# Kernel tuning notes

Hardware: AMD Instinct MI355X
Metric: run time of the kernel (lower is better)

Reference implementation:

```python
import jax, jax.numpy as jnp
import numpy as np

# ---- module hyperparameters (from init_kwargs) ----
DIST = 25
N_IN, N_HID, N_OUT = 16, 128, 2
D_MODEL, D_STATE, D_CONV, EXPAND, HEADDIM = 256, 64, 4, 2, 64
D_INNER = EXPAND * D_MODEL            # 512
NHEADS = D_INNER // HEADDIM           # 8
CONV_DIM = D_INNER + 2 * D_STATE      # 640 (x, B, C share the conv)
D_IN_PROJ = 2 * D_INNER + 2 * D_STATE + NHEADS  # 1160
NUM_CHECK = DIST ** 2 - 1             # 624 (mamba seq len)
NPG = NUM_CHECK + DIST ** 2           # 1249 nodes per graph
BATCH = 64
N_NODES = BATCH * NPG                 # 79936
N_EDGES = N_NODES * 8                 # 639488


def setup_inputs() -> dict:
    key = jax.random.key(0)
    ks = jax.random.split(key, 16)
    w = lambda k, shape, s=0.02: jax.random.normal(k, shape, jnp.float32) * s
    return {
        "node_inputs": jax.random.normal(ks[0], (N_NODES, N_IN), jnp.float32),
        "src_ids": jax.random.randint(ks[1], (N_EDGES,), 0, N_NODES),
        "dst_ids": jax.random.randint(ks[2], (N_EDGES,), 0, N_NODES),
        "W_embed": w(ks[3], (N_IN, D_MODEL)), "b_embed": jnp.zeros((D_MODEL,), jnp.float32),
        "W_in": w(ks[4], (D_MODEL, D_IN_PROJ)), "b_in": jnp.zeros((D_IN_PROJ,), jnp.float32),
        "conv_w": w(ks[5], (CONV_DIM, D_CONV), 0.1), "conv_b": jnp.zeros((CONV_DIM,), jnp.float32),
        "A_log": jnp.log(jnp.arange(1, NHEADS + 1, dtype=jnp.float32)),
        "dt_bias": w(ks[6], (NHEADS,), 0.1),
        "D_skip": jnp.ones((NHEADS,), jnp.float32),
        "norm_w": jnp.ones((D_INNER,), jnp.float32),
        "W_outp": w(ks[7], (D_INNER, D_MODEL)), "b_outp": jnp.zeros((D_MODEL,), jnp.float32),
        "W_proj": w(ks[8], (D_MODEL, N_IN)), "b_proj": jnp.zeros((N_IN,), jnp.float32),
        "W_msg": w(ks[9], (N_IN, N_HID)), "b_msg": jnp.zeros((N_HID,), jnp.float32),
        "W_upd": w(ks[10], (N_IN + N_HID, N_HID)), "b_upd": jnp.zeros((N_HID,), jnp.float32),
        "W_out": w(ks[11], (N_HID, N_OUT)), "b_out": jnp.zeros((N_OUT,), jnp.float32),
    }


def _silu(x):
    return x * jax.nn.sigmoid(x)


def _mamba2(x, W_in, b_in, conv_w, conv_b, A_log, dt_bias, D_skip, norm_w, W_outp, b_outp):
    """Mamba2 block: in_proj -> causal depthwise conv -> selective scan -> gated RMSNorm -> out_proj."""
    Bg, L, _ = x.shape
    zxbcdt = x @ W_in + b_in                       # [Bg, L, 1160]
    z = zxbcdt[..., :D_INNER]                      # gate
    xBC = zxbcdt[..., D_INNER:D_INNER + CONV_DIM]
    dt = zxbcdt[..., D_INNER + CONV_DIM:]          # [Bg, L, H]
    # causal depthwise conv over the seq dim (d_conv taps)
    xp = jnp.pad(xBC, ((0, 0), (D_CONV - 1, 0), (0, 0)))
    xBC = sum(conv_w[:, k] * xp[:, k:k + L, :] for k in range(D_CONV)) + conv_b
    xBC = _silu(xBC)
    xs = xBC[..., :D_INNER].reshape(Bg, L, NHEADS, HEADDIM)
    Bm = xBC[..., D_INNER:D_INNER + D_STATE]       # [Bg, L, N] (ngroups=1)
    Cm = xBC[..., D_INNER + D_STATE:]              # [Bg, L, N]
    dt = jax.nn.softplus(dt + dt_bias)             # [Bg, L, H]
    dA = jnp.exp(dt * (-jnp.exp(A_log)))           # [Bg, L, H]

    def step(h, inp):
        xt, Bt, Ct, dAt, dtt = inp                 # xt [Bg,H,P], Bt/Ct [Bg,N], dAt/dtt [Bg,H]
        h = dAt[..., None, None] * h + dtt[..., None, None] * xt[..., None] * Bt[:, None, None, :]
        yt = jnp.einsum('bhpn,bn->bhp', h, Ct)
        return h, yt

    h0 = jnp.zeros((Bg, NHEADS, HEADDIM, D_STATE), x.dtype)
    seq = (jnp.moveaxis(xs, 1, 0), jnp.moveaxis(Bm, 1, 0), jnp.moveaxis(Cm, 1, 0),
           jnp.moveaxis(dA, 1, 0), jnp.moveaxis(dt, 1, 0))
    _, ys = jax.lax.scan(step, h0, seq)
    ys = jnp.moveaxis(ys, 1, 0) + xs * D_skip[None, None, :, None]   # [Bg, L, H, P]
    y = ys.reshape(Bg, L, D_INNER) * _silu(z)                        # gated
    y = y * jax.lax.rsqrt(jnp.mean(y * y, axis=-1, keepdims=True) + 1e-5) * norm_w
    return y @ W_outp + b_outp


def reference(node_inputs, src_ids, dst_ids, W_embed, b_embed, W_in, b_in, conv_w, conv_b,
              A_log, dt_bias, D_skip, norm_w, W_outp, b_outp, W_proj, b_proj,
              W_msg, b_msg, W_upd, b_upd, W_out, b_out):
    # gather check-node rows: i*nodes_per_graph + j for j < num_check
    idx = (jnp.arange(BATCH)[:, None] * NPG + jnp.arange(NUM_CHECK)[None, :]).reshape(-1)
    chk = node_inputs[idx]                                           # [B*624, 16]
    emb = (chk @ W_embed + b_embed).reshape(BATCH, NUM_CHECK, D_MODEL)
    y = _mamba2(emb, W_in, b_in, conv_w, conv_b, A_log, dt_bias, D_skip, norm_w, W_outp, b_outp)
    proj = y.reshape(-1, D_MODEL) @ W_proj + b_proj                  # [B*624, 16]
    # scatter back into zero tensor at check-node slots
    feat = jnp.zeros((node_inputs.shape[0], N_IN), node_inputs.dtype).at[idx].set(proj)
    # GNN message passing: gather src, transform, scatter-sum into dst, update, readout
    msg = jax.nn.relu(feat[src_ids] @ W_msg + b_msg)                 # [E, n_hidden]
    agg = jax.ops.segment_sum(msg, dst_ids, num_segments=feat.shape[0])
    h = jax.nn.relu(jnp.concatenate([feat, agg], axis=-1) @ W_upd + b_upd)
    return h @ W_out + b_out                                         # [N, n_node_outputs]
```

## Files before the change

### kernel.cpp

```cpp
#include <hip/hip_runtime.h>
#include <math.h>

#define LSEQ 624
#define NPG_C 1249
#define BATCH_C 64
#define NROWS (BATCH_C*LSEQ)
#define N_NODES_C 79936
#define N_EDGES_C 639488
#define DIP 1160
#define DIN 512
#define CDIM 640
#define NH 8
#define HD 64
#define DS 64
#define CAP 96
#define TCH 48
#define NCHK 13
#define HSLOT 2097152

#define OFF_CHK   0
#define OFF_WF    638976
#define OFF_BF    657536
#define OFF_WOP   658944
#define OFF_BOP   667136
#define OFF_XBC   667392
#define OFF_DTV   26226432
#define OFF_EV    26545920
#define OFF_YS    26865408
#define OFF_FEAT  47312640
#define OFF_AGG   48591616
#define OFF_ECUM  (OFF_AGG + 2000000)
#define OFF_BBF   (OFF_AGG + 2400000)
#define OFF_PROJ  (OFF_XBC + 8000000)

typedef __attribute__((ext_vector_type(8))) short bf16x8;
typedef __attribute__((ext_vector_type(4))) float f32x4;

__device__ __forceinline__ float siluf(float x) {
    return x / (1.f + __expf(-x));
}

__device__ __forceinline__ unsigned short f2bf(float f) {
    unsigned int u = __float_as_uint(f);
    u += 0x7fffu + ((u >> 16) & 1u);
    return (unsigned short)(u >> 16);
}
__device__ __forceinline__ float bf2f(unsigned short h) {
    return __uint_as_float(((unsigned int)h) << 16);
}

__device__ __forceinline__ unsigned short* hstp(unsigned short* hst, int c, int b, int head) {
    return hst + (size_t)(c - 1) * HSLOT + (size_t)(b * NH + head) * 4096;
}

__global__ void k_gather(const float* __restrict__ ni, float* __restrict__ chk) {
    int gid = blockIdx.x * 256 + threadIdx.x;
    if (gid >= NROWS * 16) return;
    int row = gid >> 4, k = gid & 15;
    int node = (row / LSEQ) * NPG_C + (row % LSEQ);
    chk[gid] = ni[node * 16 + k];
}

__global__ void k_fusew(const float* __restrict__ We, const float* __restrict__ be,
                        const float* __restrict__ Wi, const float* __restrict__ bi,
                        const float* __restrict__ Wo, const float* __restrict__ bo,
                        const float* __restrict__ Wp, const float* __restrict__ bp,
                        float* __restrict__ Wf, float* __restrict__ bf,
                        float* __restrict__ Wop, float* __restrict__ bop) {
    int id = blockIdx.x * 256 + threadIdx.x;
    if (id < 16 * DIP) {
        int i = id / DIP, j = id % DIP;
        float s = 0.f;
        for (int k = 0; k < 256; k++) s = fmaf(We[i * 256 + k], Wi[k * DIP + j], s);
        Wf[id] = s;
    } else if (id < 16 * DIP + DIP) {
        int j = id - 16 * DIP;
        float s = bi[j];
        for (int k = 0; k < 256; k++) s = fmaf(be[k], Wi[k * DIP + j], s);
        bf[j] = s;
    } else if (id < 16 * DIP + DIP + DIN * 16) {
        int id2 = id - (16 * DIP + DIP);
        int c = id2 >> 4, o = id2 & 15;
        float s = 0.f;
        for (int k = 0; k < 256; k++) s = fmaf(Wo[c * 256 + k], Wp[k * 16 + o], s);
        Wop[id2] = s;
    } else if (id < 16 * DIP + DIP + DIN * 16 + 16) {
        int o = id - (16 * DIP + DIP + DIN * 16);
        float s = bp[o];
        for (int k = 0; k < 256; k++) s = fmaf(bo[k], Wp[k * 16 + o], s);
        bop[o] = s;
    }
}

__global__ __launch_bounds__(320) void k_conv(const float* __restrict__ chk,
        const float* __restrict__ Wf, const float* __restrict__ bf,
        const float* __restrict__ cw, const float* __restrict__ cb,
        float* __restrict__ xBCc, unsigned short* __restrict__ bbf) {
    int c = blockIdx.x * 320 + threadIdx.x;
    int t0 = blockIdx.y * 78;
    int b = blockIdx.z;
    float w[16];
#pragma unroll
    for (int k = 0; k < 16; k++) w[k] = Wf[k * DIP + DIN + c];
    float bfx = bf[DIN + c];
    float k0 = cw[c * 4 + 0], k1 = cw[c * 4 + 1], k2 = cw[c * 4 + 2], k3 = cw[c * 4 + 3];
    float cbv = cb[c];
    const float* crow = chk + (size_t)(b * LSEQ) * 16;
    float* out = xBCc + (size_t)(b * LSEQ) * CDIM + c;
    int isB = (c >= 512 && c < 576);
    unsigned short* bout = bbf + (size_t)(b * LSEQ) * 64 + (c - 512);

    float w0 = 0.f, w1 = 0.f, w2 = 0.f;
#pragma unroll
    for (int d = 3; d >= 1; d--) {
        int tau = t0 - d;
        float s = 0.f;
        if (tau >= 0) {
            s = bfx;
            const float* cr = crow + tau * 16;
#pragma unroll
            for (int k = 0; k < 16; k++) s = fmaf(cr[k], w[k], s);
        }
        if (d == 3) w0 = s; else if (d == 2) w1 = s; else w2 = s;
    }
    for (int t = t0; t < t0 + 78; t++) {
        const float* cr = crow + t * 16;
        float w3 = bfx;
#pragma unroll
        for (int k = 0; k < 16; k++) w3 = fmaf(cr[k], w[k], w3);
        float a = fmaf(k0, w0, fmaf(k1, w1, fmaf(k2, w2, fmaf(k3, w3, cbv))));
        float v = siluf(a);
        out[(size_t)t * CDIM] = v;
        if (isB) bout[(size_t)t * 64] = f2bf(v);
        w0 = w1; w1 = w2; w2 = w3;
    }
}

__global__ __launch_bounds__(256) void k_dte(const float* __restrict__ chk,
        const float* __restrict__ Wf, const float* __restrict__ bf,
        const float* __restrict__ A_log, const float* __restrict__ dt_bias,
        float* __restrict__ dtv, float* __restrict__ ecum) {
    int s = blockIdx.x * 4 + (threadIdx.x >> 6);
    int lane = threadIdx.x & 63;
    int h = s & 7;
    int cb = s >> 3;
    int c = cb % NCHK, b = cb / NCHK;
    int r0 = b * LSEQ + c * TCH;
    float wcol[16];
#pragma unroll
    for (int k = 0; k < 16; k++) wcol[k] = Wf[k * DIP + DIN + CDIM + h];
    float base = bf[DIN + CDIM + h] + dt_bias[h];
    float nA = -__expf(A_log[h]);
    float v = 0.f, sp = 0.f;
    if (lane < TCH) {
        const float* cr = chk + (size_t)(r0 + lane) * 16;
        float acc = base;
#pragma unroll
        for (int k = 0; k < 16; k++) acc = fmaf(cr[k], wcol[k], acc);
        sp = (acc > 20.f) ? acc : log1pf(__expf(acc));
        v = nA * sp;
    }
#pragma unroll
    for (int off = 1; off < 64; off <<= 1) {
        float u = __shfl_up(v, off);
        if (lane >= off) v += u;
    }
    if (lane < TCH) {
        dtv[(size_t)(r0 + lane) * NH + h] = sp;
        ecum[(size_t)(r0 + lane) * NH + h] = v;
    }
}

__global__ __launch_bounds__(256) void k_gmat(const float* __restrict__ xBCc,
        float* __restrict__ Gm) {
    int c = blockIdx.x, b = blockIdx.y;
    int tid = threadIdx.x;
    int bs = b * LSEQ;
    __shared__ __align__(16) float sBC[TCH * 132];
#pragma unroll
    for (int j = 0; j < 6; j++) {
        int g = j * 256 + tid;
        int f = g * 4;
        int t = f >> 7, col = f & 127;
        float4 v = *(const float4*)(xBCc + (size_t)(bs + c * TCH + t) * CDIM + 512 + col);
        *(float4*)&sBC[t * 132 + col] = v;
    }
    __syncthreads();
    int t0 = (tid >> 4) * 3, s0 = (tid & 15) * 3;
    float acc[3][3];
#pragma unroll
    for (int i = 0; i < 3; i++)
#pragma unroll
        for (int j = 0; j < 3; j++) acc[i][j] = 0.f;
    for (int k = 0; k < 64; k++) {
        float c0 = sBC[(t0 + 0) * 132 + 64 + k];
        float c1 = sBC[(t0 + 1) * 132 + 64 + k];
        float c2 = sBC[(t0 + 2) * 132 + 64 + k];
        float b0 = sBC[(s0 + 0) * 132 + k];
        float b1 = sBC[(s0 + 1) * 132 + k];
        float b2 = sBC[(s0 + 2) * 132 + k];
        acc[0][0] = fmaf(c0, b0, acc[0][0]); acc[0][1] = fmaf(c0, b1, acc[0][1]); acc[0][2] = fmaf(c0, b2, acc[0][2]);
        acc[1][0] = fmaf(c1, b0, acc[1][0]); acc[1][1] = fmaf(c1, b1, acc[1][1]); acc[1][2] = fmaf(c1, b2, acc[1][2]);
        acc[2][0] = fmaf(c2, b0, acc[2][0]); acc[2][1] = fmaf(c2, b1, acc[2][1]); acc[2][2] = fmaf(c2, b2, acc[2][2]);
    }
    size_t gb = (size_t)(b * NCHK + c) * (TCH * TCH);
#pragma unroll
    for (int i = 0; i < 3; i++)
#pragma unroll
        for (int j = 0; j < 3; j++)
            Gm[gb + (t0 + i) * TCH + (s0 + j)] = acc[i][j];
}

__global__ __launch_bounds__(256) void k_scarry(const float* __restrict__ xBCc,
        const unsigned short* __restrict__ bbf,
        const float* __restrict__ dtv, const float* __restrict__ ecum,
        unsigned short* __restrict__ hst) {
    int head = blockIdx.x, b = blockIdx.y;
    int pz = blockIdx.z * 32;
    int tid = threadIdx.x;
    int bs = b * LSEQ;
    __shared__ __align__(16) float sX[TCH * 32];
    __shared__ __align__(16) float sB[TCH * 64];
    __shared__ float sW[TCH];

    int i2 = (tid >> 4) * 2;
    int j4 = (tid & 15) * 4;

    float h[2][4];
#pragma unroll
    for (int i = 0; i < 2; i++)
#pragma unroll
        for (int j = 0; j < 4; j++) h[i][j] = 0.f;

    float4 rX0, rX1;
    ushort4 rBu[3];
    float rEc = 0.f, rDt = 0.f, rEcL = 0.f;

#define SC_ISSUE(cc)                                                                \
    {                                                                               \
        int r0i = bs + (cc) * TCH;                                                  \
        {   int f = 4 * tid; int t = f >> 5; int col = f & 31;                      \
            rX0 = *(const float4*)(xBCc + (size_t)(r0i + t) * CDIM + head * HD + pz + col); \
            if (tid < 128) {                                                        \
                int f2 = 1024 + 4 * tid; int t2 = f2 >> 5; int col2 = f2 & 31;      \
                rX1 = *(const float4*)(xBCc + (size_t)(r0i + t2) * CDIM + head * HD + pz + col2); \
            }                                                                       \
        }                                                                           \
        _Pragma("unroll")                                                           \
        for (int jj = 0; jj < 3; jj++) {                                            \
            int g = jj * 256 + tid; int f = 4 * g; int t = f >> 6; int col = f & 63;\
            rBu[jj] = *(const ushort4*)(bbf + (size_t)(r0i + t) * 64 + col);        \
        }                                                                           \
        if (tid < TCH) { rEc = ecum[(size_t)(r0i + tid) * NH + head];               \
                         rDt = dtv[(size_t)(r0i + tid) * NH + head]; }              \
        rEcL = ecum[(size_t)(r0i + TCH - 1) * NH + head];                           \
    }

    SC_ISSUE(0);
    for (int c = 0; c < NCHK; c++) {
        __syncthreads();
        float eL = __expf(rEcL);
        {
            int f = 4 * tid;
            *(float4*)&sX[f] = rX0;
            if (tid < 128) *(float4*)&sX[1024 + f] = rX1;
        }
#pragma unroll
        for (int jj = 0; jj < 3; jj++) {
            int g = jj * 256 + tid;
            float4 bv = { bf2f(rBu[jj].x), bf2f(rBu[jj].y), bf2f(rBu[jj].z), bf2f(rBu[jj].w) };
            *(float4*)&sB[4 * g] = bv;
        }
        if (tid < TCH) sW[tid] = __expf(rEcL - rEc) * rDt;
        __syncthreads();
        if (c + 1 < NCHK) SC_ISSUE(c + 1);

        if (c > 0) {
            unsigned short* hp = hstp(hst, c, b, head);
#pragma unroll
            for (int ii = 0; ii < 2; ii++) {
                ushort4 v = { f2bf(h[ii][0]), f2bf(h[ii][1]), f2bf(h[ii][2]), f2bf(h[ii][3]) };
                *(ushort4*)&hp[(pz + i2 + ii) * 64 + j4] = v;
            }
        }

#pragma unroll
        for (int i = 0; i < 2; i++)
#pragma unroll
            for (int j = 0; j < 4; j++) h[i][j] *= eL;
        for (int s = 0; s < TCH; s++) {
            float w = sW[s];
            float2 xv = *(const float2*)&sX[s * 32 + i2];
            float4 bv = *(const float4*)&sB[s * 64 + j4];
            float x0 = w * xv.x, x1 = w * xv.y;
            h[0][0] = fmaf(x0, bv.x, h[0][0]); h[0][1] = fmaf(x0, bv.y, h[0][1]);
            h[0][2] = fmaf(x0, bv.z, h[0][2]); h[0][3] = fmaf(x0, bv.w, h[0][3]);
            h[1][0] = fmaf(x1, bv.x, h[1][0]); h[1][1] = fmaf(x1, bv.y, h[1][1]);
            h[1][2] = fmaf(x1, bv.z, h[1][2]); h[1][3] = fmaf(x1, bv.w, h[1][3]);
        }
    }
#undef SC_ISSUE
}

__global__ __launch_bounds__(256) void k_intra(float* __restrict__ xBCc,
        const float* __restrict__ Gm, const float* __restrict__ dtv,
        const float* __restrict__ ecum, const float* __restrict__ Dskip,
        const unsigned short* __restrict__ hst) {
    int bid = blockIdx.x;
    int xcd = bid & 7;
    int head = (bid >> 3) & 7;
    int g = (bid >> 6) * 8 + xcd;
    int c = g % NCHK, b = g / NCHK;
    int tid = threadIdx.x;
    int lane = tid & 63;
    int wv = tid >> 6;
    int bs = b * LSEQ;
    int r0 = bs + c * TCH;

    __shared__ __align__(16) unsigned char smraw[35904];
    float* sXf = (float*)(smraw);
    unsigned short* sMh = (unsigned short*)(smraw + 12288);
    unsigned short* sMl = (unsigned short*)(smraw + 19200);
    unsigned short* sCt = (unsigned short*)(smraw + 19200);
    unsigned short* sXh = (unsigned short*)(smraw + 26112);
    unsigned short* sHt = (unsigned short*)(smraw + 26112);
    float* sE  = (float*)(smraw + 35328);
    float* sEx = (float*)(smraw + 35520);
    float* sdt = (float*)(smraw + 35712);

    ushort4 rHu[4];
    if (c > 0) {
        const unsigned short* hp = hstp((unsigned short*)hst, c, b, head);
#pragma unroll
        for (int j = 0; j < 4; j++)
            rHu[j] = *(const ushort4*)(hp + 4 * (j * 256 + tid));
    }

    ushort4 rCu[3];
#pragma unroll
    for (int j = 0; j < 3; j++) {
        int g2 = j * 256 + tid;
        int t = g2 >> 4, col = (g2 & 15) * 4;
        const float* rowp = xBCc + (size_t)(r0 + t) * CDIM;
        float4 xv = *(const float4*)(rowp + head * HD + col);
        *(float4*)&sXf[t * 64 + col] = xv;
        float4 cv = *(const float4*)(rowp + 576 + col);
        ushort4 cu = { f2bf(cv.x), f2bf(cv.y), f2bf(cv.z), f2bf(cv.w) };
        rCu[j] = cu;
    }
    if (tid < TCH) {
        float e = ecum[(size_t)(r0 + tid) * NH + head];
        sE[tid] = e;
        sEx[tid] = __expf(e);
        sdt[tid] = dtv[(size_t)(r0 + tid) * NH + head];
    }
    __syncthreads();

    size_t gb = (size_t)(b * NCHK + c) * (TCH * TCH);
#pragma unroll
    for (int k = 0; k < 9; k++) {
        int id = k * 256 + tid;
        int t = id / TCH, s = id - t * TCH;
        float gv = Gm[gb + id];
        float m = (s <= t) ? __expf(sE[t] - sE[s]) * sdt[s] * gv : 0.f;
        unsigned short mh = f2bf(m);
        sMh[t * 72 + s] = mh;
        sMl[t * 72 + s] = f2bf(m - bf2f(mh));
    }
    for (int w = tid; w < 768; w += 256) {
        int t = w >> 4, s = 48 + (w & 15);
        sMh[t * 72 + s] = 0;
        sMl[t * 72 + s] = 0;
    }
#pragma unroll
    for (int i = 0; i < 3; i++) {
        int w = i * 256 + tid;
        int p = w & 63, k4 = (w >> 6) * 4;
        float v0 = sXf[(k4 + 0) * 64 + p];
        float v1 = sXf[(k4 + 1) * 64 + p];
        float v2 = sXf[(k4 + 2) * 64 + p];
        float v3 = sXf[(k4 + 3) * 64 + p];
        ushort4 hi = { f2bf(v0), f2bf(v1), f2bf(v2), f2bf(v3) };
        *(ushort4*)&sXh[p * 72 + k4] = hi;
    }
    {
        int p = tid >> 2, k4 = 48 + (tid & 3) * 4;
        ushort4 z = { 0, 0, 0, 0 };
        *(ushort4*)&sXh[p * 72 + k4] = z;
    }
    __syncthreads();

    int pt = wv * 16;
    int colL = lane & 15;
    int rbase = (lane >> 4) * 4;
    int kfrag = 8 * (lane >> 4);

    float xo[3][4];
#pragma unroll
    for (int tt = 0; tt < 3; tt++)
#pragma unroll
        for (int r = 0; r < 4; r++)
            xo[tt][r] = sXf[(tt * 16 + rbase + r) * 64 + pt + colL];

    f32x4 acc[3] = { {0,0,0,0}, {0,0,0,0}, {0,0,0,0} };
    f32x4 acc2[3] = { {0,0,0,0}, {0,0,0,0}, {0,0,0,0} };
#pragma unroll
    for (int ks = 0; ks < 64; ks += 32) {
        bf16x8 bh = *(const bf16x8*)&sXh[(pt + colL) * 72 + ks + kfrag];
#pragma unroll
        for (int tt = 0; tt < 3; tt++) {
            bf16x8 ah = *(const bf16x8*)&sMh[(tt * 16 + colL) * 72 + ks + kfrag];
            bf16x8 al = *(const bf16x8*)&sMl[(tt * 16 + colL) * 72 + ks + kfrag];
            acc[tt] = __builtin_amdgcn_mfma_f32_16x16x32_bf16(ah, bh, acc[tt], 0, 0, 0);
            acc[tt] = __builtin_amdgcn_mfma_f32_16x16x32_bf16(al, bh, acc[tt], 0, 0, 0);
        }
    }
    __syncthreads();
#pragma unroll
    for (int j = 0; j < 3; j++) {
        int g2 = j * 256 + tid;
        int t = g2 >> 4, col = (g2 & 15) * 4;
        *(ushort4*)&sCt[t * 72 + col] = rCu[j];
    }
    if (c > 0) {
#pragma unroll
        for (int j = 0; j < 4; j++) {
            int e = 4 * (j * 256 + tid);
            int p = e >> 6, n4 = e & 63;
            *(ushort4*)&sHt[p * 72 + n4] = rHu[j];
        }
    }
    __syncthreads();
    if (c > 0) {
#pragma unroll
        for (int ks = 0; ks < 64; ks += 32) {
            bf16x8 bhh = *(const bf16x8*)&sHt[(pt + colL) * 72 + ks + kfrag];
#pragma unroll
            for (int tt = 0; tt < 3; tt++) {
                bf16x8 ac = *(const bf16x8*)&sCt[(tt * 16 + colL) * 72 + ks + kfrag];
                acc2[tt] = __builtin_amdgcn_mfma_f32_16x16x32_bf16(ac, bhh, acc2[tt], 0, 0, 0);
            }
        }
    }

    float dsk = Dskip[head];
#pragma unroll
    for (int tt = 0; tt < 3; tt++) {
#pragma unroll
        for (int r = 0; r < 4; r++) {
            int trow = tt * 16 + rbase + r;
            float y = fmaf(dsk, xo[tt][r], acc[tt][r]);
            if (c > 0) y = fmaf(sEx[trow], acc2[tt][r], y);
            xBCc[(size_t)(r0 + trow) * CDIM + head * HD + pt + colL] = y;
        }
    }
}

__global__ __launch_bounds__(256) void k_gate(const float* __restrict__ chk,
        const float* __restrict__ Wf, const float* __restrict__ bf,
        const float* __restrict__ ysx, const float* __restrict__ norm_w,
        const float* __restrict__ Wop, const float* __restrict__ bop,
        float* __restrict__ feat) {
    int row0 = blockIdx.x * 8;
    int tid = threadIdx.x;
    __shared__ float sy[2][512];
    __shared__ float sred[2][256];
    __shared__ float swave[2][4];
    int c1 = tid, c2 = tid + 256;
    float wz1[16], wz2[16];
#pragma unroll
    for (int k = 0; k < 16; k++) {
        wz1[k] = Wf[k * DIP + c1];
        wz2[k] = Wf[k * DIP + c2];
    }
    float zb1 = bf[c1], zb2 = bf[c2];
    float nw1 = norm_w[c1], nw2 = norm_w[c2];
    int o = tid & 15, kg = tid >> 4;
    int wid = tid >> 6, lane = tid & 63;

    for (int g2 = 0; g2 < 4; g2++) {
        int rb = row0 + g2 * 2;
        float gn1[2], gn2[2];
#pragma unroll
        for (int r = 0; r < 2; r++) {
            int row = rb + r;
            const float4* cp = (const float4*)(chk + (size_t)row * 16);
            float4 cA = cp[0], cB = cp[1], cC = cp[2], cD = cp[3];
            float cv[16] = {cA.x,cA.y,cA.z,cA.w, cB.x,cB.y,cB.z,cB.w,
                            cC.x,cC.y,cC.z,cC.w, cD.x,cD.y,cD.z,cD.w};
            float z1 = zb1, z2 = zb2;
#pragma unroll
            for (int k = 0; k < 16; k++) {
                z1 = fmaf(cv[k], wz1[k], z1);
                z2 = fmaf(cv[k], wz2[k], z2);
            }
            float y1 = ysx[(size_t)row * CDIM + c1] * siluf(z1);
            float y2 = ysx[(size_t)row * CDIM + c2] * siluf(z2);
            gn1[r] = y1;
            gn2[r] = y2;
            float ss = y1 * y1 + y2 * y2;
#pragma unroll
            for (int off = 32; off >= 1; off >>= 1) ss += __shfl_xor(ss, off);
            if (lane == 0) swave[r][wid] = ss;
        }
        __syncthreads();
#pragma unroll
        for (int r = 0; r < 2; r++) {
            float tot = swave[r][0] + swave[r][1] + swave[r][2] + swave[r][3];
            float scale = 1.f / sqrtf(tot * (1.f / 512.f) + 1e-5f);
            sy[r][c1] = gn1[r] * scale * nw1;
            sy[r][c2] = gn2[r] * scale * nw2;
        }
        __syncthreads();
#pragma unroll
        for (int r = 0; r < 2; r++) {
            float ps = 0.f;
#pragma unroll
            for (int j = 0; j < 32; j++) {
                int k = kg * 32 + j;
                ps = fmaf(sy[r][k], Wop[k * 16 + o], ps);
            }
            sred[r][kg * 16 + o] = ps;
        }
        __syncthreads();
        if (tid < 32) {
            int r = tid >> 4, oo = tid & 15;
            float s = bop[oo];
#pragma unroll
            for (int g = 0; g < 16; g++) s += sred[r][g * 16 + oo];
            int row = rb + r;
            int bb = row / LSEQ, t = row % LSEQ;
            feat[(size_t)(bb * NPG_C + t) * 16 + oo] = s;
        }
    }
}

__global__ void k_scatter(const int* __restrict__ src, const int* __restrict__ dst,
                          int* __restrict__ cnt, int* __restrict__ slots) {
    int e = blockIdx.x * 256 + threadIdx.x;
    if (e >= N_EDGES_C) return;
    int d = dst[e];
    int pos = atomicAdd(&cnt[d], 1);
    if (pos < CAP) slots[(size_t)d * CAP + pos] = src[e];
}

__global__ __launch_bounds__(256) void k_proj(const float* __restrict__ feat,
        const float* __restrict__ Wm, const float* __restrict__ bm,
        unsigned short* __restrict__ p) {
    int tid = threadIdx.x;
    int c = tid & 127, half = tid >> 7;
    float w[16];
#pragma unroll
    for (int k = 0; k < 16; k++) w[k] = Wm[k * 128 + c];
    float bmv = bm[c];
    int base = blockIdx.x * 8;
#pragma unroll
    for (int q = 0; q < 4; q++) {
        int node = base + q * 2 + half;
        const float4* fr = (const float4*)(feat + (size_t)node * 16);
        float4 f0 = fr[0], f1 = fr[1], f2 = fr[2], f3 = fr[3];
        float m = bmv;
        m = fmaf(f0.x, w[0],  m); m = fmaf(f0.y, w[1],  m);
        m = fmaf(f0.z, w[2],  m); m = fmaf(f0.w, w[3],  m);
        m = fmaf(f1.x, w[4],  m); m = fmaf(f1.y, w[5],  m);
        m = fmaf(f1.z, w[6],  m); m = fmaf(f1.w, w[7],  m);
        m = fmaf(f2.x, w[8],  m); m = fmaf(f2.y, w[9],  m);
        m = fmaf(f2.z, w[10], m); m = fmaf(f2.w, w[11], m);
        m = fmaf(f3.x, w[12], m); m = fmaf(f3.y, w[13], m);
        m = fmaf(f3.z, w[14], m); m = fmaf(f3.w, w[15], m);
        p[(size_t)node * 128 + c] = f2bf(fmaxf(m, 0.f));
    }
}

__global__ __launch_bounds__(256) void k_agg2(const int* __restrict__ cnt,
        const int* __restrict__ slots, const unsigned short* __restrict__ p,
        float* __restrict__ agg) {
    int wid = threadIdx.x >> 6, lane = threadIdx.x & 63;
    int esub = lane >> 4, cl = lane & 15;
    int d = blockIdx.x * 4 + wid;
    int deg = cnt[d];
    if (deg > CAP) deg = CAP;
    const int* sl = slots + (size_t)d * CAP;

    float acc[8];
#pragma unroll
    for (int j = 0; j < 8; j++) acc[j] = 0.f;

    int e = esub;
    int s = (e < deg) ? sl[e] : -1;
    while (e < deg) {
        int scur = s;
        int en = e + 4;
        if (en < deg) s = sl[en];
        ushort4 v0, v1;
        {
            const unsigned short* pp = p + (size_t)scur * 128 + cl * 8;
            v0 = *(const ushort4*)(pp);
            v1 = *(const ushort4*)(pp + 4);
        }
        acc[0] += bf2f(v0.x); acc[1] += bf2f(v0.y);
        acc[2] += bf2f(v0.z); acc[3] += bf2f(v0.w);
        acc[4] += bf2f(v1.x); acc[5] += bf2f(v1.y);
        acc[6] += bf2f(v1.z); acc[7] += bf2f(v1.w);
        e = en;
    }
#pragma unroll
    for (int j = 0; j < 8; j++) {
        acc[j] += __shfl_xor(acc[j], 16);
        acc[j] += __shfl_xor(acc[j], 32);
    }
    if (esub == 0) {
        float4 o0 = { acc[0], acc[1], acc[2], acc[3] };
        float4 o1 = { acc[4], acc[5], acc[6], acc[7] };
        float* ap = agg + (size_t)d * 128 + cl * 8;
        *(float4*)(ap) = o0;
        *(float4*)(ap + 4) = o1;
    }
}

#define UNB 32
__global__ __launch_bounds__(256) void k_upd2(const float* __restrict__ feat,
        const float* __restrict__ agg, const float* __restrict__ Wu,
        const float* __restrict__ bu, const float* __restrict__ Wo2,
        const float* __restrict__ bo2, float* __restrict__ out) {
    int g0 = blockIdx.x * UNB;
    int tid = threadIdx.x;
    __shared__ __align__(16) float sin_[UNB][144];
    __shared__ float part[4][8][2];
    for (int w = tid; w < UNB * 144; w += 256) {
        int node = w / 144, k = w - node * 144;
        sin_[node][k] = (k < 16) ? feat[(size_t)(g0 + node) * 16 + k]
                                 : agg[(size_t)(g0 + node) * 128 + (k - 16)];
    }
    __syncthreads();
    int c6 = tid & 63;
    int grp = tid >> 6;
    float acc[8][2];
#pragma unroll
    for (int nn = 0; nn < 8; nn++) { acc[nn][0] = 0.f; acc[nn][1] = 0.f; }

    for (int k0 = 0; k0 < 144; k0 += 4) {
        float wA0 = Wu[(k0 + 0) * 128 + c6], wB0 = Wu[(k0 + 0) * 128 + 64 + c6];
        float wA1 = Wu[(k0 + 1) * 128 + c6], wB1 = Wu[(k0 + 1) * 128 + 64 + c6];
        float wA2 = Wu[(k0 + 2) * 128 + c6], wB2 = Wu[(k0 + 2) * 128 + 64 + c6];
        float wA3 = Wu[(k0 + 3) * 128 + c6], wB3 = Wu[(k0 + 3) * 128 + 64 + c6];
#pragma unroll
        for (int nn = 0; nn < 8; nn++) {
            float4 s4 = *(const float4*)&sin_[grp * 8 + nn][k0];
            acc[nn][0] = fmaf(s4.x, wA0, acc[nn][0]);
            acc[nn][1] = fmaf(s4.x, wB0, acc[nn][1]);
            acc[nn][0] = fmaf(s4.y, wA1, acc[nn][0]);
            acc[nn][1] = fmaf(s4.y, wB1, acc[nn][1]);
            acc[nn][0] = fmaf(s4.z, wA2, acc[nn][0]);
            acc[nn][1] = fmaf(s4.z, wB2, acc[nn][1]);
            acc[nn][0] = fmaf(s4.w, wA3, acc[nn][0]);
            acc[nn][1] = fmaf(s4.w, wB3, acc[nn][1]);
        }
    }

    float buA = bu[c6], buB = bu[64 + c6];
    float2 woA = *(const float2*)&Wo2[c6 * 2];
    float2 woB = *(const float2*)&Wo2[(64 + c6) * 2];
    float p[8][2];
#pragma unroll
    for (int nn = 0; nn < 8; nn++) {
        float h0 = fmaxf(acc[nn][0] + buA, 0.f);
        float h1 = fmaxf(acc[nn][1] + buB, 0.f);
        p[nn][0] = h0 * woA.x + h1 * woB.x;
        p[nn][1] = h0 * woA.y + h1 * woB.y;
    }
#pragma unroll
    for (int off = 1; off < 64; off <<= 1) {
#pragma unroll
        for (int nn = 0; nn < 8; nn++) {
            p[nn][0] += __shfl_xor(p[nn][0], off);
            p[nn][1] += __shfl_xor(p[nn][1], off);
        }
    }
    if ((tid & 63) == 0) {
#pragma unroll
        for (int nn = 0; nn < 8; nn++) {
            part[grp][nn][0] = p[nn][0];
            part[grp][nn][1] = p[nn][1];
        }
    }
    __syncthreads();
    if (tid < 64) {
        int node = tid >> 1, o = tid & 1;
        out[(size_t)(g0 + node) * 2 + o] = part[node >> 3][node & 7][o] + bo2[o];
    }
}

extern "C" void kernel_launch(void* const* d_in, const int* in_sizes, int n_in,
                              void* d_out, int out_size, void* d_ws, size_t ws_size,
                              hipStream_t stream) {
    const float* node_inputs = (const float*)d_in[0];
    const int*   src_ids     = (const int*)d_in[1];
    const int*   dst_ids     = (const int*)d_in[2];
    const float* W_embed     = (const float*)d_in[3];
    const float* b_embed     = (const float*)d_in[4];
    const float* W_in        = (const float*)d_in[5];
    const float* b_in        = (const float*)d_in[6];
    const float* conv_w      = (const float*)d_in[7];
    const float* conv_b      = (const float*)d_in[8];
    const float* A_log       = (const float*)d_in[9];
    const float* dt_bias     = (const float*)d_in[10];
    const float* D_skip      = (const float*)d_in[11];
    const float* norm_w      = (const float*)d_in[12];
    const float* W_outp      = (const float*)d_in[13];
    const float* b_outp      = (const float*)d_in[14];
    const float* W_proj      = (const float*)d_in[15];
    const float* b_proj      = (const float*)d_in[16];
    const float* W_msg       = (const float*)d_in[17];
    const float* b_msg       = (const float*)d_in[18];
    const float* W_upd       = (const float*)d_in[19];
    const float* b_upd       = (const float*)d_in[20];
    const float* W_out       = (const float*)d_in[21];
    const float* b_out       = (const float*)d_in[22];

    float* ws   = (float*)d_ws;
    float* chk  = ws + OFF_CHK;
    float* Wf   = ws + OFF_WF;
    float* bf   = ws + OFF_BF;
    float* Wop  = ws + OFF_WOP;
    float* bop  = ws + OFF_BOP;
    float* xBCc = ws + OFF_XBC;
    float* dtv  = ws + OFF_DTV;
    float* ecum = ws + OFF_ECUM;
    unsigned short* hst = (unsigned short*)(ws + OFF_YS);
    unsigned short* bbf = (unsigned short*)(ws + OFF_BBF);
    float* feat = ws + OFF_FEAT;
    float* agg  = ws + OFF_AGG;
    float* Gm   = ws + OFF_AGG;
    unsigned short* pmsg = (unsigned short*)(ws + OFF_PROJ);
    int*   slots = (int*)(ws + OFF_XBC);
    int*   cnt   = (int*)(ws + OFF_DTV);
    float* out  = (float*)d_out;

    hipMemsetAsync(feat, 0, (size_t)N_NODES_C * 16 * 4, stream);

    k_gather<<<(NROWS * 16 + 255) / 256, 256, 0, stream>>>(node_inputs, chk);
    k_fusew<<<(16 * DIP + DIP + DIN * 16 + 16 + 255) / 256, 256, 0, stream>>>(
        W_embed, b_embed, W_in, b_in, W_outp, b_outp, W_proj, b_proj, Wf, bf, Wop, bop);
    k_conv<<<dim3(2, 8, BATCH_C), 320, 0, stream>>>(chk, Wf, bf, conv_w, conv_b, xBCc, bbf);
    k_dte<<<(BATCH_C * NCHK * NH) / 4, 256, 0, stream>>>(chk, Wf, bf, A_log, dt_bias, dtv, ecum);
    k_gmat<<<dim3(NCHK, BATCH_C), 256, 0, stream>>>(xBCc, Gm);
    k_scarry<<<dim3(NH, BATCH_C, 2), 256, 0, stream>>>(xBCc, bbf, dtv, ecum, hst);
    k_intra<<<NCHK * NH * BATCH_C, 256, 0, stream>>>(xBCc, Gm, dtv, ecum, D_skip, hst);
    k_gate<<<NROWS / 8, 256, 0, stream>>>(chk, Wf, bf, xBCc, norm_w, Wop, bop, feat);
    hipMemsetAsync(cnt, 0, (size_t)N_NODES_C * 4, stream);
    k_scatter<<<(N_EDGES_C + 255) / 256, 256, 0, stream>>>(src_ids, dst_ids, cnt, slots);
    k_proj<<<N_NODES_C / 8, 256, 0, stream>>>(feat, W_msg, b_msg, pmsg);
    k_agg2<<<N_NODES_C / 4, 256, 0, stream>>>(cnt, slots, pmsg, agg);
    k_upd2<<<N_NODES_C / UNB, 256, 0, stream>>>(feat, agg, W_upd, b_upd, W_out, b_out, out);
}
```

Measured before the change: 395.7 us.

## Compute chunk state carry with bf16 MFMA using hi/lo split of x

Rewrites the inter-chunk state recurrence kernel so the per-chunk outer-product accumulation runs on 16x16x32 bf16 MFMA instructions instead of scalar FMAs. The weighted x values are split into high and low bf16 parts to approximate fp32 accuracy, and tiles are stored transposed in shared memory with zero-padded K. The grid drops its z split, so each block now covers a full head (64x64 state) with four waves. This trades more shared-memory traffic and half the blocks for much higher matmul throughput, with a small precision change.

```diff
diff --git a/kernel.cpp b/kernel.cpp
--- a/kernel.cpp
+++ b/kernel.cpp
@@ -216,87 +216,96 @@
         const float* __restrict__ dtv, const float* __restrict__ ecum,
         unsigned short* __restrict__ hst) {
     int head = blockIdx.x, b = blockIdx.y;
-    int pz = blockIdx.z * 32;
     int tid = threadIdx.x;
+    int lane = tid & 63, wv = tid >> 6;
     int bs = b * LSEQ;
-    __shared__ __align__(16) float sX[TCH * 32];
-    __shared__ __align__(16) float sB[TCH * 64];
-    __shared__ float sW[TCH];
-
-    int i2 = (tid >> 4) * 2;
-    int j4 = (tid & 15) * 4;
-
-    float h[2][4];
-#pragma unroll
-    for (int i = 0; i < 2; i++)
-#pragma unroll
-        for (int j = 0; j < 4; j++) h[i][j] = 0.f;
-
-    float4 rX0, rX1;
+    __shared__ unsigned short sXh[64 * 72];
+    __shared__ unsigned short sXl[64 * 72];
+    __shared__ unsigned short sBn[64 * 72];
+
+    int colL = lane & 15;
+    int rbase = (lane >> 4) * 4;
+    int kfrag = 8 * (lane >> 4);
+
+    f32x4 acc[4] = { {0,0,0,0}, {0,0,0,0}, {0,0,0,0}, {0,0,0,0} };
+
+    float4 rX[3];
     ushort4 rBu[3];
-    float rEc = 0.f, rDt = 0.f, rEcL = 0.f;
+    float rEc[3], rDt[3], rEcL = 0.f;
 
 #define SC_ISSUE(cc)                                                                \
     {                                                                               \
         int r0i = bs + (cc) * TCH;                                                  \
-        {   int f = 4 * tid; int t = f >> 5; int col = f & 31;                      \
-            rX0 = *(const float4*)(xBCc + (size_t)(r0i + t) * CDIM + head * HD + pz + col); \
-            if (tid < 128) {                                                        \
-                int f2 = 1024 + 4 * tid; int t2 = f2 >> 5; int col2 = f2 & 31;      \
-                rX1 = *(const float4*)(xBCc + (size_t)(r0i + t2) * CDIM + head * HD + pz + col2); \
-            }                                                                       \
-        }                                                                           \
         _Pragma("unroll")                                                           \
         for (int jj = 0; jj < 3; jj++) {                                            \
-            int g = jj * 256 + tid; int f = 4 * g; int t = f >> 6; int col = f & 63;\
+            int g = jj * 256 + tid; int t = g >> 4; int col = (g & 15) * 4;         \
+            rX[jj] = *(const float4*)(xBCc + (size_t)(r0i + t) * CDIM + head * HD + col); \
             rBu[jj] = *(const ushort4*)(bbf + (size_t)(r0i + t) * 64 + col);        \
+            rEc[jj] = ecum[(size_t)(r0i + t) * NH + head];                          \
+            rDt[jj] = dtv[(size_t)(r0i + t) * NH + head];                           \
         }                                                                           \
-        if (tid < TCH) { rEc = ecum[(size_t)(r0i + tid) * NH + head];               \
-                         rDt = dtv[(size_t)(r0i + tid) * NH + head]; }              \
         rEcL = ecum[(size_t)(r0i + TCH - 1) * NH + head];                           \
+    }
+
+    {
+        int p = tid >> 2, k4 = 48 + (tid & 3) * 4;
+        ushort4 z = { 0, 0, 0, 0 };
+        *(ushort4*)&sXh[p * 72 + k4] = z;
+        *(ushort4*)&sXl[p * 72 + k4] = z;
+        *(ushort4*)&sBn[p * 72 + k4] = z;
     }
 
     SC_ISSUE(0);
     for (int c = 0; c < NCHK; c++) {
         __syncthreads();
         float eL = __expf(rEcL);
-        {
-            int f = 4 * tid;
-            *(float4*)&sX[f] = rX0;
-            if (tid < 128) *(float4*)&sX[1024 + f] = rX1;
-        }
 #pragma unroll
         for (int jj = 0; jj < 3; jj++) {
             int g = jj * 256 + tid;
-            float4 bv = { bf2f(rBu[jj].x), bf2f(rBu[jj].y), bf2f(rBu[jj].z), bf2f(rBu[jj].w) };
-            *(float4*)&sB[4 * g] = bv;
-        }
-        if (tid < TCH) sW[tid] = __expf(rEcL - rEc) * rDt;
+            int t = g >> 4, col = (g & 15) * 4;
+            float w = __expf(rEcL - rEc[jj]) * rDt[jj];
+            float m0 = w * rX[jj].x, m1 = w * rX[jj].y;
+            float m2 = w * rX[jj].z, m3 = w * rX[jj].w;
+            unsigned short h0 = f2bf(m0), h1 = f2bf(m1), h2 = f2bf(m2), h3 = f2bf(m3);
+            sXh[(col + 0) * 72 + t] = h0;
+            sXh[(col + 1) * 72 + t] = h1;
+            sXh[(col + 2) * 72 + t] = h2;
+            sXh[(col + 3) * 72 + t] = h3;
+            sXl[(col + 0) * 72 + t] = f2bf(m0 - bf2f(h0));
+            sXl[(col + 1) * 72 + t] = f2bf(m1 - bf2f(h1));
+            sXl[(col + 2) * 72 + t] = f2bf(m2 - bf2f(h2));
+            sXl[(col + 3) * 72 + t] = f2bf(m3 - bf2f(h3));
+            sBn[(col + 0) * 72 + t] = rBu[jj].x;
+            sBn[(col + 1) * 72 + t] = rBu[jj].y;
+            sBn[(col + 2) * 72 + t] = rBu[jj].z;
+            sBn[(col + 3) * 72 + t] = rBu[jj].w;
+        }
         __syncthreads();
         if (c + 1 < NCHK) SC_ISSUE(c + 1);
 
         if (c > 0) {
             unsigned short* hp = hstp(hst, c, b, head);
 #pragma unroll
-            for (int ii = 0; ii < 2; ii++) {
-                ushort4 v = { f2bf(h[ii][0]), f2bf(h[ii][1]), f2bf(h[ii][2]), f2bf(h[ii][3]) };
-                *(ushort4*)&hp[(pz + i2 + ii) * 64 + j4] = v;
+            for (int nt = 0; nt < 4; nt++)
+#pragma unroll
+                for (int r = 0; r < 4; r++)
+                    hp[(wv * 16 + rbase + r) * 64 + nt * 16 + colL] = f2bf(acc[nt][r]);
+        }
+#pragma unroll
+        for (int nt = 0; nt < 4; nt++)
+#pragma unroll
+            for (int r = 0; r < 4; r++)
+                acc[nt][r] *= eL;
+#pragma unroll
+        for (int ks = 0; ks < 64; ks += 32) {
+            bf16x8 ah = *(const bf16x8*)&sXh[(wv * 16 + colL) * 72 + ks + kfrag];
+            bf16x8 al = *(const bf16x8*)&sXl[(wv * 16 + colL) * 72 + ks + kfrag];
+#pragma unroll
+            for (int nt = 0; nt < 4; nt++) {
+                bf16x8 bb = *(const bf16x8*)&sBn[(nt * 16 + colL) * 72 + ks + kfrag];
+                acc[nt] = __builtin_amdgcn_mfma_f32_16x16x32_bf16(ah, bb, acc[nt], 0, 0, 0);
+                acc[nt] = __builtin_amdgcn_mfma_f32_16x16x32_bf16(al, bb, acc[nt], 0, 0, 0);
             }
-        }
-
-#pragma unroll
-        for (int i = 0; i < 2; i++)
-#pragma unroll
-            for (int j = 0; j < 4; j++) h[i][j] *= eL;
-        for (int s = 0; s < TCH; s++) {
-            float w = sW[s];
-            float2 xv = *(const float2*)&sX[s * 32 + i2];
-            float4 bv = *(const float4*)&sB[s * 64 + j4];
-            float x0 = w * xv.x, x1 = w * xv.y;
-            h[0][0] = fmaf(x0, bv.x, h[0][0]); h[0][1] = fmaf(x0, bv.y, h[0][1]);
-            h[0][2] = fmaf(x0, bv.z, h[0][2]); h[0][3] = fmaf(x0, bv.w, h[0][3]);
-            h[1][0] = fmaf(x1, bv.x, h[1][0]); h[1][1] = fmaf(x1, bv.y, h[1][1]);
-            h[1][2] = fmaf(x1, bv.z, h[1][2]); h[1][3] = fmaf(x1, bv.w, h[1][3]);
         }
     }
 #undef SC_ISSUE
@@ -745,7 +754,7 @@
     k_conv<<<dim3(2, 8, BATCH_C), 320, 0, stream>>>(chk, Wf, bf, conv_w, conv_b, xBCc, bbf);
     k_dte<<<(BATCH_C * NCHK * NH) / 4, 256, 0, stream>>>(chk, Wf, bf, A_log, dt_bias, dtv, ecum);
     k_gmat<<<dim3(NCHK, BATCH_C), 256, 0, stream>>>(xBCc, Gm);
-    k_scarry<<<dim3(NH, BATCH_C, 2), 256, 0, stream>>>(xBCc, bbf, dtv, ecum, hst);
+    k_scarry<<<dim3(NH, BATCH_C), 256, 0, stream>>>(xBCc, bbf, dtv, ecum, hst);
     k_intra<<<NCHK * NH * BATCH_C, 256, 0, stream>>>(xBCc, Gm, dtv, ecum, D_skip, hst);
     k_gate<<<NROWS / 8, 256, 0, stream>>>(chk, Wf, bf, xBCc, norm_w, Wop, bop, feat);
     hipMemsetAsync(cnt, 0, (size_t)N_NODES_C * 4, stream);
```

After: 380.6 us. -3.8%, faster.
